# Kernel tuning notes

Hardware: AMD Instinct MI355X
Metric: run time of the kernel (lower is better)

The kernel has to match this reference:

```python
import jax, jax.numpy as jnp
import numpy as np

B, T, I, R, O = 128, 512, 64, 512, 64

def setup_inputs() -> dict:
    key = jax.random.key(0)
    ks = jax.random.split(key, 6)
    s = lambda fan_in: 1.0 / np.sqrt(fan_in)
    return {
        "x_pred": jax.random.normal(ks[0], (B, T, I), dtype=jnp.float32),
        "h0": jnp.zeros((B, R), dtype=jnp.float32),
        "W_h": jax.random.uniform(ks[1], (R, R), jnp.float32, -s(R), s(R)),
        "b_h": jax.random.uniform(ks[2], (R,), jnp.float32, -s(R), s(R)),
        "U_h": jax.random.uniform(ks[3], (R, I), jnp.float32, -s(I), s(I)),
        "W_out": jax.random.uniform(ks[4], (O, R), jnp.float32, -s(R), s(R)),
        "b_out": jax.random.uniform(ks[5], (O,), jnp.float32, -s(R), s(R)),
    }

def reference(x_pred, h0, W_h, b_h, U_h, W_out, b_out):
    # Precompute input projections for all timesteps: [T, B, R]
    u = jnp.einsum('bti,ri->tbr', x_pred, U_h)

    def step(x, u_t):
        # x: [B, R] hidden state; u_t: [B, R]
        x = jnp.tanh(x @ W_h.T + b_h + u_t)
        y_t = x @ W_out.T + b_out  # [B, O]
        return x, y_t

    x_last, y = jax.lax.scan(step, h0, u)
    y = jnp.transpose(y, (1, 0, 2))  # [B, T, O]
    return y, (x_last, x_last)
```

## Files before the change

### kernel.cpp

```cpp
#include <hip/hip_runtime.h>

#define B_ 128
#define T_ 512
#define I_ 64
#define R_ 512
#define O_ 64
#define NG 8
#define GB 16

typedef _Float16 f16;
typedef __attribute__((ext_vector_type(8))) _Float16 half8;
typedef __attribute__((ext_vector_type(4))) float f32x4;

#define MFMA16 __builtin_amdgcn_mfma_f32_16x16x32_f16

#define NLW 15
#define NRW 49
#define WLDS_BYTES (8 * NLW * 1024)
#define HOFF WLDS_BYTES
#define HBYTES 16384
#define SMEM_TOTAL (WLDS_BYTES + 2 * HBYTES)

__device__ __forceinline__ float tanh_fast(float x) {
    float e = __expf(2.0f * x);
    return 1.0f - 2.0f * __builtin_amdgcn_rcpf(e + 1.0f);
}

__device__ __forceinline__ half8 cvt_h8(const float4 a, const float4 b) {
    half8 r;
    r[0] = (f16)a.x; r[1] = (f16)a.y; r[2] = (f16)a.z; r[3] = (f16)a.w;
    r[4] = (f16)b.x; r[5] = (f16)b.y; r[6] = (f16)b.z; r[7] = (f16)b.w;
    return r;
}

__device__ __forceinline__ unsigned pack2(float a, float b) {
    union { f16 h[2]; unsigned u; } r;
    r.h[0] = (f16)a; r.h[1] = (f16)b; return r.u;
}

__global__ void __launch_bounds__(256) pre_kernel(
    const float* __restrict__ x_pred, const float* __restrict__ b_h,
    const float* __restrict__ U_h, f16* __restrict__ ubuf)
{
    const int tid = threadIdx.x;
    const int w = tid >> 6, l = tid & 63, lg = l >> 4, ln = l & 15;
    const int g = blockIdx.x & 7, tc = blockIdx.x >> 3;
    const int b0 = g * GB;

    half8 uf[8][2];
    float4 bh4[8];
    #pragma unroll
    for (int j = 0; j < 8; ++j) {
        const int rt = 128 * w + 16 * j;
        bh4[j] = *(const float4*)(b_h + rt + 4 * lg);
        #pragma unroll
        for (int ks = 0; ks < 2; ++ks) {
            const float* p = U_h + (size_t)(rt + ln) * I_ + 32 * ks + 8 * lg;
            uf[j][ks] = cvt_h8(*(const float4*)p, *(const float4*)(p + 4));
        }
    }
    for (int tt = 0; tt < 4; ++tt) {
        const int t = tc * 4 + tt;
        half8 xf[2];
        #pragma unroll
        for (int ks = 0; ks < 2; ++ks) {
            const float* p = x_pred + ((size_t)(b0 + ln) * T_ + t) * I_ + 32 * ks + 8 * lg;
            xf[ks] = cvt_h8(*(const float4*)p, *(const float4*)(p + 4));
        }
        char* ut = (char*)ubuf + (size_t)(t * NG + g) * 16384;
        #pragma unroll
        for (int j = 0; j < 8; ++j) {
            f32x4 acc = {0.f, 0.f, 0.f, 0.f};
            acc = MFMA16(uf[j][0], xf[0], acc, 0, 0, 0);
            acc = MFMA16(uf[j][1], xf[1], acc, 0, 0, 0);
            const int rt = 128 * w + 16 * j;
            uint2 pk;
            pk.x = pack2(acc[0] + bh4[j].x, acc[1] + bh4[j].y);
            pk.y = pack2(acc[2] + bh4[j].z, acc[3] + bh4[j].w);
            *(uint2*)(ut + ln * 1024 + 2 * (rt + 4 * lg)) = pk;
        }
    }
}

__global__ void __launch_bounds__(512, 2) rnn_kernel(
    const float* __restrict__ h0, const float* __restrict__ W_h,
    f16* __restrict__ uh, float* __restrict__ out)
{
    extern __shared__ char smem[];
    const int tid = threadIdx.x;
    const int w = tid >> 6, l = tid & 63, lg = l >> 4, ln = l & 15;
    const int g = blockIdx.x;
    const int b0 = g * GB;
    const int rw = w * 64;

    half8 wfr[NRW];
    #pragma unroll
    for (int j = 0; j < 4; ++j) {
        const float* wr = W_h + (size_t)(rw + 16 * j + ln) * R_;
        #pragma unroll
        for (int ks = 0; ks < 16; ++ks) {
            const float* p = wr + 32 * ks + 8 * lg;
            half8 f = cvt_h8(*(const float4*)p, *(const float4*)(p + 4));
            const int fi = ks * 4 + j;
            if (fi < NLW) *(half8*)(smem + ((w * NLW + fi) << 10) + (l << 4)) = f;
            else wfr[fi - NLW] = f;
        }
    }
    {
        const int b = tid >> 5, r0 = (tid & 31) * 16;
        const int sb = (b & 7) << 4;
        const float* hp = h0 + (size_t)(b0 + b) * R_ + r0;
        #pragma unroll
        for (int q = 0; q < 4; ++q) {
            float4 v = *(const float4*)(hp + 4 * q);
            uint2 pk;
            pk.x = pack2(v.x, v.y); pk.y = pack2(v.z, v.w);
            *(uint2*)(smem + HOFF + b * 1024 + ((2 * (r0 + 4 * q)) ^ sb)) = pk;
        }
    }
    uint2 uu[4];
    #pragma unroll
    for (int j = 0; j < 4; ++j)
        uu[j] = *(const uint2*)((char*)uh + (size_t)g * 16384 + ln * 1024 + 2 * (rw + 16 * j + 4 * lg));
    __syncthreads();

    const int asb = (ln & 7) << 4;

    #pragma unroll 1
    for (int t = 0; t < T_; ++t) {
        char* hc = smem + HOFF + (t & 1) * HBYTES;
        char* hn = smem + HOFF + ((t & 1) ^ 1) * HBYTES;
        char* slot = (char*)uh + (size_t)(t * NG + g) * 16384;
        const bool lastt = (t == T_ - 1);

        f32x4 acc[4];
        #pragma unroll
        for (int j = 0; j < 4; ++j) {
            union { uint2 u; f16 h[4]; } c; c.u = uu[j];
            acc[j] = (f32x4){(float)c.h[0], (float)c.h[1], (float)c.h[2], (float)c.h[3]};
        }
        if (!lastt) {
            const char* un = (const char*)uh + (size_t)((t + 1) * NG + g) * 16384;
            #pragma unroll
            for (int j = 0; j < 4; ++j)
                uu[j] = *(const uint2*)(un + ln * 1024 + 2 * (rw + 16 * j + 4 * lg));
        }
        #pragma unroll
        for (int ks = 0; ks < 16; ++ks) {
            half8 hb = *(const half8*)(hc + ln * 1024 + ((64 * ks + 16 * lg) ^ asb));
            #pragma unroll
            for (int j = 0; j < 4; ++j) {
                const int fi = ks * 4 + j;
                half8 aa;
                if (fi < NLW) aa = *(const half8*)(smem + ((w * NLW + fi) << 10) + (l << 4));
                else aa = wfr[fi - NLW];
                acc[j] = MFMA16(aa, hb, acc[j], 0, 0, 0);
            }
        }
        #pragma unroll
        for (int j = 0; j < 4; ++j) {
            const int rb = 2 * (rw + 16 * j + 4 * lg);
            float v0 = tanh_fast(acc[j][0]), v1 = tanh_fast(acc[j][1]);
            float v2 = tanh_fast(acc[j][2]), v3 = tanh_fast(acc[j][3]);
            uint2 pk;
            pk.x = pack2(v0, v1); pk.y = pack2(v2, v3);
            *(uint2*)(slot + ln * 1024 + rb) = pk;
            if (!lastt) {
                *(uint2*)(hn + ln * 1024 + (rb ^ asb)) = pk;
            } else {
                float* xd = out + (size_t)B_ * T_ * O_ + (size_t)(b0 + ln) * R_ + (rw + 16 * j + 4 * lg);
                float4 xv = make_float4(v0, v1, v2, v3);
                *(float4*)xd = xv;
                *(float4*)(xd + (size_t)B_ * R_) = xv;
            }
        }
        asm volatile("s_waitcnt lgkmcnt(0)\n\ts_barrier" ::: "memory");
    }
}

__global__ void __launch_bounds__(256) y_kernel(
    const f16* __restrict__ hbuf, const float* __restrict__ W_out,
    const float* __restrict__ b_out, float* __restrict__ out)
{
    const int tid = threadIdx.x;
    const int w = tid >> 6, l = tid & 63, lg = l >> 4, ln = l & 15;
    const int g = blockIdx.x & 7, tc = blockIdx.x >> 3;
    const int b0 = g * GB;

    half8 wf[16];
    #pragma unroll
    for (int ks = 0; ks < 16; ++ks) {
        const float* p = W_out + (size_t)(16 * w + ln) * R_ + 32 * ks + 8 * lg;
        wf[ks] = cvt_h8(*(const float4*)p, *(const float4*)(p + 4));
    }
    const float bo = b_out[16 * w + ln];

    for (int tt = 0; tt < 4; ++tt) {
        const int t = tc * 4 + tt;
        const char* hb = (const char*)hbuf + (size_t)(t * NG + g) * 16384;
        f32x4 acc = {0.f, 0.f, 0.f, 0.f};
        #pragma unroll
        for (int ks = 0; ks < 16; ++ks) {
            half8 a = *(const half8*)(hb + ln * 1024 + 64 * ks + 16 * lg);
            acc = MFMA16(a, wf[ks], acc, 0, 0, 0);
        }
        #pragma unroll
        for (int q = 0; q < 4; ++q) {
            const int b = 4 * lg + q;
            out[((size_t)(b0 + b) * T_ + t) * O_ + 16 * w + ln] = acc[q] + bo;
        }
    }
}

extern "C" void kernel_launch(void* const* d_in, const int* in_sizes, int n_in,
                              void* d_out, int out_size, void* d_ws, size_t ws_size,
                              hipStream_t stream) {
    const float* x_pred = (const float*)d_in[0];
    const float* h0     = (const float*)d_in[1];
    const float* W_h    = (const float*)d_in[2];
    const float* b_h    = (const float*)d_in[3];
    const float* U_h    = (const float*)d_in[4];
    const float* W_out  = (const float*)d_in[5];
    const float* b_out  = (const float*)d_in[6];
    float* out = (float*)d_out;

    f16* ubuf = (f16*)d_ws;

    hipFuncSetAttribute(reinterpret_cast<const void*>(rnn_kernel),
                        hipFuncAttributeMaxDynamicSharedMemorySize, SMEM_TOTAL);

    pre_kernel<<<dim3(NG * 128), dim3(256), 0, stream>>>(x_pred, b_h, U_h, ubuf);
    rnn_kernel<<<dim3(NG), dim3(512), SMEM_TOTAL, stream>>>(h0, W_h, ubuf, out);
    y_kernel<<<dim3(NG * 128), dim3(256), 0, stream>>>(ubuf, W_out, b_out, out);
}
```

Baseline: 1.914 ms.

## Replace per-step block barrier with per-wave LDS flags and staggered K-slice order

Removes the workgroup-wide s_barrier at the end of each timestep. Each wave now publishes a completion counter in LDS, and consumers poll only the producer wave whose hidden-state slice they are about to read. The K-loop order is rotated per wave so each wave starts on its own freshly written slice, and later slices are checked incrementally, letting waves drift apart instead of lockstepping. The weight register/LDS split is reorganized so that the j=3 fragments come from LDS. This risks spin-wait overhead, and correctness depends on the ordering of LDS writes against the flag store. The next-buffer overwrite hazard relies on the double buffer and on the chain of dependencies between waves.

```diff
diff --git a/kernel.cpp b/kernel.cpp
--- a/kernel.cpp
+++ b/kernel.cpp
@@ -15,11 +15,11 @@
 #define MFMA16 __builtin_amdgcn_mfma_f32_16x16x32_f16
 
 #define NLW 15
-#define NRW 49
 #define WLDS_BYTES (8 * NLW * 1024)
 #define HOFF WLDS_BYTES
 #define HBYTES 16384
-#define SMEM_TOTAL (WLDS_BYTES + 2 * HBYTES)
+#define FLGOFF (HOFF + 2 * HBYTES)
+#define SMEM_TOTAL (FLGOFF + 64)
 
 __device__ __forceinline__ float tanh_fast(float x) {
     float e = __expf(2.0f * x);
@@ -93,17 +93,20 @@
     const int b0 = g * GB;
     const int rw = w * 64;
 
-    half8 wfr[NRW];
-    #pragma unroll
-    for (int j = 0; j < 4; ++j) {
-        const float* wr = W_h + (size_t)(rw + 16 * j + ln) * R_;
-        #pragma unroll
-        for (int ks = 0; ks < 16; ++ks) {
-            const float* p = wr + 32 * ks + 8 * lg;
+    if (tid < 8) *(int*)(smem + FLGOFF + tid * 4) = 0;
+
+    half8 wfr[49];
+    #pragma unroll
+    for (int i = 0; i < 16; ++i) {
+        const int ks = (2 * w + i) & 15;
+        #pragma unroll
+        for (int j = 0; j < 4; ++j) {
+            const float* p = W_h + (size_t)(rw + 16 * j + ln) * R_ + 32 * ks + 8 * lg;
             half8 f = cvt_h8(*(const float4*)p, *(const float4*)(p + 4));
-            const int fi = ks * 4 + j;
-            if (fi < NLW) *(half8*)(smem + ((w * NLW + fi) << 10) + (l << 4)) = f;
-            else wfr[fi - NLW] = f;
+            if (j == 3) {
+                if (i < 15) *(half8*)(smem + ((w * NLW + i) << 10) + (l << 4)) = f;
+                else wfr[48] = f;
+            } else wfr[i * 3 + j] = f;
         }
     }
     {
@@ -125,13 +128,17 @@
     __syncthreads();
 
     const int asb = (ln & 7) << 4;
+    volatile const int* vf = (volatile const int*)(smem + FLGOFF);
 
     #pragma unroll 1
     for (int t = 0; t < T_; ++t) {
-        char* hc = smem + HOFF + (t & 1) * HBYTES;
+        const char* hbp = smem + HOFF + (t & 1) * HBYTES + ln * 1024;
         char* hn = smem + HOFF + ((t & 1) ^ 1) * HBYTES;
         char* slot = (char*)uh + (size_t)(t * NG + g) * 16384;
         const bool lastt = (t == T_ - 1);
+        unsigned hoff_dyn = 0;
+
+        int fA = vf[(w + 1) & 7], fB = vf[(w + 2) & 7], fC = vf[(w + 3) & 7], fD = vf[(w + 4) & 7];
 
         f32x4 acc[4];
         #pragma unroll
@@ -145,18 +152,47 @@
             for (int j = 0; j < 4; ++j)
                 uu[j] = *(const uint2*)(un + ln * 1024 + 2 * (rw + 16 * j + 4 * lg));
         }
-        #pragma unroll
-        for (int ks = 0; ks < 16; ++ks) {
-            half8 hb = *(const half8*)(hc + ln * 1024 + ((64 * ks + 16 * lg) ^ asb));
-            #pragma unroll
-            for (int j = 0; j < 4; ++j) {
-                const int fi = ks * 4 + j;
-                half8 aa;
-                if (fi < NLW) aa = *(const half8*)(smem + ((w * NLW + fi) << 10) + (l << 4));
-                else aa = wfr[fi - NLW];
-                acc[j] = MFMA16(aa, hb, acc[j], 0, 0, 0);
-            }
-        }
+
+        #define CHECK(c_, fvar) do {                                           \
+            int fv_ = fvar;                                                    \
+            if (fv_ < t) {                                                     \
+                volatile const int* pp_ = vf + ((w + (c_)) & 7);               \
+                do { fv_ = *pp_; } while (fv_ < t);                            \
+            }                                                                  \
+            asm volatile("" : "+v"(hoff_dyn) : "v"(fv_));                      \
+        } while (0)
+
+        #define SLICE(i_) do {                                                 \
+            const int ks_ = (2 * w + (i_)) & 15;                               \
+            const half8 hb_ = *(const half8*)(hbp + hoff_dyn +                 \
+                ((unsigned)(64 * ks_ + 16 * lg) ^ (unsigned)asb));             \
+            half8 a3_;                                                         \
+            if ((i_) < 15) a3_ = *(const half8*)(smem + ((w * NLW + (i_)) << 10) + (l << 4)); \
+            else a3_ = wfr[48];                                                \
+            acc[0] = MFMA16(wfr[(i_) * 3 + 0], hb_, acc[0], 0, 0, 0);          \
+            acc[1] = MFMA16(wfr[(i_) * 3 + 1], hb_, acc[1], 0, 0, 0);          \
+            acc[2] = MFMA16(wfr[(i_) * 3 + 2], hb_, acc[2], 0, 0, 0);          \
+            acc[3] = MFMA16(a3_, hb_, acc[3], 0, 0, 0);                        \
+        } while (0)
+
+        SLICE(0); SLICE(1);
+        CHECK(1, fA); fA = vf[(w + 5) & 7];
+        SLICE(2); SLICE(3);
+        CHECK(2, fB); fB = vf[(w + 6) & 7];
+        SLICE(4); SLICE(5);
+        CHECK(3, fC); fC = vf[(w + 7) & 7];
+        SLICE(6); SLICE(7);
+        CHECK(4, fD);
+        SLICE(8); SLICE(9);
+        CHECK(5, fA);
+        SLICE(10); SLICE(11);
+        CHECK(6, fB);
+        SLICE(12); SLICE(13);
+        CHECK(7, fC);
+        SLICE(14); SLICE(15);
+        #undef SLICE
+        #undef CHECK
+
         #pragma unroll
         for (int j = 0; j < 4; ++j) {
             const int rb = 2 * (rw + 16 * j + 4 * lg);
@@ -174,7 +210,10 @@
                 *(float4*)(xd + (size_t)B_ * R_) = xv;
             }
         }
-        asm volatile("s_waitcnt lgkmcnt(0)\n\ts_barrier" ::: "memory");
+        if (!lastt) {
+            asm volatile("s_waitcnt lgkmcnt(0)" ::: "memory");
+            if (l == 0) *(volatile int*)(smem + FLGOFF + w * 4) = t + 1;
+        }
     }
 }
 
```

Result: slower. 2.570 ms (+34.3%).
